# Optimization experiments

Measured on AMD Instinct MI355X. Metric: run time of the kernel, lower is better.

The kernel has to match this reference:

```python
import jax, jax.numpy as jnp
import numpy as np

N = 50000      # nodes
E = 800000     # edges (avg degree 16)
F_IN = 128     # input_dim
HID = 64       # hidden_dim
HEADS = 4      # heads on first layer only
G = 512        # number of graphs in batch
EPS = 1e-5
NEG_SLOPE = 0.2

# (in_dim, out_dim, heads) per GATv2 layer
LAYER_DIMS = [(F_IN, HID, HEADS), (HID * HEADS, HID, 1), (HID, HID, 1)]


def setup_inputs() -> dict:
    key = jax.random.key(0)
    ks = jax.random.split(key, 16)
    def rn(k, shape, fan_in):
        return jax.random.normal(k, shape, jnp.float32) / np.float32(np.sqrt(fan_in))
    inp = {}
    inp["x"] = jax.random.normal(ks[0], (N, F_IN), jnp.float32)
    inp["edge_index"] = jax.random.randint(ks[1], (2, E), 0, N)
    inp["batch"] = jnp.sort(jax.random.randint(ks[2], (N,), 0, G))
    i = 3
    for l, (din, dout, h) in enumerate(LAYER_DIMS):
        kk = jax.random.split(ks[i], 3)
        inp[f"Wl{l}"] = rn(kk[0], (din, h * dout), din)
        inp[f"bl{l}"] = jnp.zeros((h * dout,), jnp.float32)
        inp[f"Wr{l}"] = rn(kk[1], (din, h * dout), din)
        inp[f"br{l}"] = jnp.zeros((h * dout,), jnp.float32)
        inp[f"att{l}"] = rn(kk[2], (h, dout), dout)
        inp[f"bias{l}"] = jnp.zeros((h * dout,), jnp.float32)
        inp[f"ln_g{l}"] = jnp.ones((h * dout,), jnp.float32)
        inp[f"ln_b{l}"] = jnp.zeros((h * dout,), jnp.float32)
        i += 1
    inp["Wh1"] = rn(ks[i], (HID, HID), HID)
    inp["bh1"] = jnp.zeros((HID,), jnp.float32)
    inp["Wh2"] = rn(ks[i + 1], (HID, 1), HID)
    inp["bh2"] = jnp.zeros((1,), jnp.float32)
    return inp


def gatv2_layer(x, src, dst, Wl, bl, Wr, br, att, bias, heads, out_c):
    """PyG GATv2Conv (concat=True, share_weights=False, eval mode)."""
    n = x.shape[0]
    xl = (x @ Wl + bl).reshape(n, heads, out_c)   # messages (source side)
    xr = (x @ Wr + br).reshape(n, heads, out_c)   # destination side
    e = jax.nn.leaky_relu(xl[src] + xr[dst], NEG_SLOPE)          # [E,H,C]
    logit = jnp.einsum('ehc,hc->eh', e, att)                      # [E,H]
    m = jax.ops.segment_max(logit, dst, num_segments=n)           # segment-softmax
    ex = jnp.exp(logit - m[dst])
    den = jax.ops.segment_sum(ex, dst, num_segments=n)
    alpha = ex / den[dst]                                         # [E,H]
    out = jax.ops.segment_sum(alpha[:, :, None] * xl[src], dst, num_segments=n)
    return out.reshape(n, heads * out_c) + bias


def graph_layernorm(h, g, b):
    """PyG LayerNorm(mode='graph') with batch=None: normalize over all elements."""
    mu = h.mean()
    xc = h - mu
    var = (xc * xc).mean()
    return xc * jax.lax.rsqrt(var + EPS) * g + b


def reference(x, edge_index, batch,
              Wl0, bl0, Wr0, br0, att0, bias0, ln_g0, ln_b0,
              Wl1, bl1, Wr1, br1, att1, bias1, ln_g1, ln_b1,
              Wl2, bl2, Wr2, br2, att2, bias2, ln_g2, ln_b2,
              Wh1, bh1, Wh2, bh2):
    src, dst = edge_index[0], edge_index[1]
    layers = [
        (Wl0, bl0, Wr0, br0, att0, bias0, ln_g0, ln_b0),
        (Wl1, bl1, Wr1, br1, att1, bias1, ln_g1, ln_b1),
        (Wl2, bl2, Wr2, br2, att2, bias2, ln_g2, ln_b2),
    ]
    h = x
    for (Wl, bl, Wr, br, att, bias, g, b), (_, dout, heads) in zip(layers, LAYER_DIMS):
        h_in = h
        h = gatv2_layer(h, src, dst, Wl, bl, Wr, br, att, bias, heads, dout)
        h = graph_layernorm(h, g, b)
        h = jax.nn.relu(h)
        if h_in.shape[1] == h.shape[1]:   # residual only when widths match
            h = h + h_in
        # dropout: identity in eval mode
    # global mean pool over graphs
    counts = jax.ops.segment_sum(jnp.ones((h.shape[0], 1), h.dtype), batch, num_segments=G)
    Z = jax.ops.segment_sum(h, batch, num_segments=G) / jnp.maximum(counts, 1.0)
    logits = jax.nn.relu(Z @ Wh1 + bh1) @ Wh2 + bh2
    return logits
```

## Files before the change

### kernel.cpp

```cpp
#include <hip/hip_runtime.h>
#include <math.h>

#define NN 50000
#define NE 800000
#define NG 512
#define LRELU 0.2f
#define LN_EPS 1e-5
#define GCAP 128
#define NBUCK 256

typedef __attribute__((ext_vector_type(8))) short short8;
typedef __attribute__((ext_vector_type(4))) float f32x4;

__global__ void hist_kernel(const int* __restrict__ dst, int* __restrict__ deg) {
    int e = blockIdx.x * blockDim.x + threadIdx.x;
    if (e < NE) atomicAdd(&deg[dst[e]], 1);
}

__global__ __launch_bounds__(1024) void scan1(const int* __restrict__ deg,
                                              int* __restrict__ excl,
                                              int* __restrict__ bsum, int n) {
    __shared__ int s[1024];
    int tid = threadIdx.x;
    int gid = blockIdx.x * 1024 + tid;
    int v = (gid < n) ? deg[gid] : 0;
    s[tid] = v;
    __syncthreads();
    for (int off = 1; off < 1024; off <<= 1) {
        int t = (tid >= off) ? s[tid - off] : 0;
        __syncthreads();
        s[tid] += t;
        __syncthreads();
    }
    if (gid < n) excl[gid] = s[tid] - v;
    if (tid == 1023) bsum[blockIdx.x] = s[1023];
}

__global__ __launch_bounds__(64) void scan2(int* __restrict__ bsum, int nb) {
    int lane = threadIdx.x;
    int v = (lane < nb) ? bsum[lane] : 0;
    int orig = v;
    #pragma unroll
    for (int off = 1; off < 64; off <<= 1) {
        int t = __shfl_up(v, off, 64);
        if (lane >= off) v += t;
    }
    if (lane < nb) bsum[lane] = v - orig;
}

__global__ __launch_bounds__(1024) void scan3(int* __restrict__ row_ptr,
                                              int* __restrict__ cursor,
                                              const int* __restrict__ bsum, int n) {
    int tid = threadIdx.x;
    int gid = blockIdx.x * 1024 + tid;
    if (gid < n) {
        int v = row_ptr[gid] + bsum[blockIdx.x];
        row_ptr[gid] = v;
        cursor[gid] = v;
    }
    if (gid == 0) row_ptr[n] = NE;
}

__global__ void scatter_kernel(const int* __restrict__ src, const int* __restrict__ dst,
                               int* __restrict__ cursor, int* __restrict__ col_src) {
    int e = blockIdx.x * blockDim.x + threadIdx.x;
    if (e < NE) {
        int pos = atomicAdd(&cursor[dst[e]], 1);
        col_src[pos] = src[e];
    }
}

__device__ inline void split_bf16(float v, ushort& h, ushort& l) {
    unsigned ub = __float_as_uint(v);
    unsigned hh = (ub + 0x7FFFu + ((ub >> 16) & 1u)) >> 16;
    float vh = __uint_as_float(hh << 16);
    float r = v - vh;
    unsigned ur = __float_as_uint(r);
    unsigned ll = (ur + 0x7FFFu + ((ur >> 16) & 1u)) >> 16;
    h = (ushort)hh; l = (ushort)ll;
}

__global__ __launch_bounds__(256) void prep_w(const float* __restrict__ Wl0,
                                              const float* __restrict__ Wr0,
                                              const float* __restrict__ Wl1,
                                              const float* __restrict__ Wr1,
                                              const float* __restrict__ Wl2,
                                              const float* __restrict__ Wr2,
                                              ushort* __restrict__ wt) {
    int id = blockIdx.x * 256 + threadIdx.x;
    const float* W; int K, N, rel; ushort* hi;
    if (id < 65536) {
        W = (id < 32768) ? Wl0 : Wr0;
        rel = id & 32767; K = 128; N = 256;
        hi = wt + ((id < 32768) ? 0 : 65536);
    } else if (id < 98304) {
        int t = id - 65536;
        W = (t < 16384) ? Wl1 : Wr1;
        rel = t & 16383; K = 256; N = 64;
        hi = wt + 131072 + ((t < 16384) ? 0 : 32768);
    } else if (id < 106496) {
        int t = id - 98304;
        W = (t < 4096) ? Wl2 : Wr2;
        rel = t & 4095; K = 64; N = 64;
        hi = wt + 196608 + ((t < 4096) ? 0 : 8192);
    } else return;
    ushort* lo = hi + K * N;
    int n = rel / K, k = rel - n * K;
    ushort h, l;
    split_bf16(W[k * N + n], h, l);
    hi[rel] = h;
    lo[rel] = l;
}

__global__ __launch_bounds__(256) void gemm_mfma(const float* __restrict__ A,
                                                 const ushort* __restrict__ Bhi,
                                                 const ushort* __restrict__ Blo,
                                                 const float* __restrict__ bias,
                                                 float* __restrict__ C,
                                                 int M, int Ncol, int K,
                                                 const float* __restrict__ lnstats,
                                                 const float* __restrict__ lng,
                                                 const float* __restrict__ lnb) {
    __shared__ ushort sAh[64][40];
    __shared__ ushort sAl[64][40];
    __shared__ ushort sBh[64][40];
    __shared__ ushort sBl[64][40];
    const int tid = threadIdx.x;
    const int row0 = blockIdx.x * 64;
    const int col0 = blockIdx.y * 64;
    const int w = tid >> 6, lane = tid & 63;
    const int fm = lane & 15;
    const int fk = (lane >> 4) * 8;
    const bool doln = (lnstats != nullptr);
    float mu = 0.f, rstd = 0.f;
    if (doln) { mu = lnstats[0]; rstd = lnstats[1]; }
    f32x4 acc[4] = {};

    for (int k0 = 0; k0 < K; k0 += 32) {
        __syncthreads();
        int f = tid;
        #pragma unroll
        for (int it = 0; it < 2; it++, f += 256) {
            int r = f >> 3, kc = (f & 7) * 4;
            int grow = row0 + r;
            float4 v = (grow < M) ? *(const float4*)&A[(size_t)grow * K + k0 + kc]
                                  : make_float4(0.f, 0.f, 0.f, 0.f);
            if (doln) {
                int c0 = k0 + kc;
                v.x = fmaxf((v.x - mu) * rstd * lng[c0 + 0] + lnb[c0 + 0], 0.f);
                v.y = fmaxf((v.y - mu) * rstd * lng[c0 + 1] + lnb[c0 + 1], 0.f);
                v.z = fmaxf((v.z - mu) * rstd * lng[c0 + 2] + lnb[c0 + 2], 0.f);
                v.w = fmaxf((v.w - mu) * rstd * lng[c0 + 3] + lnb[c0 + 3], 0.f);
            }
            ushort4 h, l;
            split_bf16(v.x, h.x, l.x);
            split_bf16(v.y, h.y, l.y);
            split_bf16(v.z, h.z, l.z);
            split_bf16(v.w, h.w, l.w);
            *(ushort4*)&sAh[r][kc] = h;
            *(ushort4*)&sAl[r][kc] = l;
        }
        int u = tid;
        #pragma unroll
        for (int it = 0; it < 2; it++, u += 256) {
            int n = u >> 3, kc = (u & 7) * 4;
            *(ushort4*)&sBh[n][kc] = *(const ushort4*)&Bhi[(size_t)(col0 + n) * K + k0 + kc];
            *(ushort4*)&sBl[n][kc] = *(const ushort4*)&Blo[(size_t)(col0 + n) * K + k0 + kc];
        }
        __syncthreads();
        short8 ah = *(const short8*)&sAh[w * 16 + fm][fk];
        short8 al = *(const short8*)&sAl[w * 16 + fm][fk];
        #pragma unroll
        for (int c = 0; c < 4; c++) {
            short8 bh = *(const short8*)&sBh[c * 16 + fm][fk];
            short8 bl = *(const short8*)&sBl[c * 16 + fm][fk];
            acc[c] = __builtin_amdgcn_mfma_f32_16x16x32_bf16(ah, bh, acc[c], 0, 0, 0);
            acc[c] = __builtin_amdgcn_mfma_f32_16x16x32_bf16(al, bh, acc[c], 0, 0, 0);
            acc[c] = __builtin_amdgcn_mfma_f32_16x16x32_bf16(ah, bl, acc[c], 0, 0, 0);
        }
    }
    const int orow = w * 16 + (lane >> 4) * 4;
    #pragma unroll
    for (int c = 0; c < 4; c++) {
        int col = col0 + c * 16 + fm;
        float bv = bias[col];
        #pragma unroll
        for (int r = 0; r < 4; r++) {
            int grow = row0 + orow + r;
            if (grow < M) C[(size_t)grow * Ncol + col] = acc[c][r] + bv;
        }
    }
}

__global__ __launch_bounds__(256) void gat4(const float* __restrict__ xl,
                                            const float* __restrict__ xr,
                                            const float* __restrict__ att,
                                            const float* __restrict__ bias,
                                            const int* __restrict__ row_ptr,
                                            const int* __restrict__ col_src,
                                            float* __restrict__ out,
                                            double* __restrict__ red) {
    __shared__ int scol[4][GCAP];
    __shared__ double bs1[4], bs2[4];
    const int tid = threadIdx.x;
    const int w = tid >> 6, lane = tid & 63;
    const int n = blockIdx.x * 4 + w;
    const int base = row_ptr[n];
    int deg = row_ptr[n + 1] - base;
    if (deg > GCAP) deg = GCAP;
    for (int j = lane; j < deg; j += 64) scol[w][j] = col_src[base + j];
    const float4 rxr  = ((const float4*)(xr + (size_t)n * 256))[lane];
    const float4 ratt = ((const float4*)att)[lane];
    __syncthreads();

    float m = -1e30f, sum = 0.f;
    float4 acc = {0.f, 0.f, 0.f, 0.f};
    float4 xvn = {0.f, 0.f, 0.f, 0.f};
    if (deg > 0) xvn = ((const float4*)(xl + (size_t)scol[w][0] * 256))[lane];
    for (int j = 0; j < deg; j++) {
        float4 xv = xvn;
        if (j + 1 < deg) xvn = ((const float4*)(xl + (size_t)scol[w][j + 1] * 256))[lane];
        float vx = xv.x + rxr.x; vx = (vx > 0.f) ? vx : LRELU * vx;
        float vy = xv.y + rxr.y; vy = (vy > 0.f) ? vy : LRELU * vy;
        float vz = xv.z + rxr.z; vz = (vz > 0.f) ? vz : LRELU * vz;
        float vw = xv.w + rxr.w; vw = (vw > 0.f) ? vw : LRELU * vw;
        float p = vx * ratt.x + vy * ratt.y + vz * ratt.z + vw * ratt.w;
        p += __shfl_xor(p, 1, 64);
        p += __shfl_xor(p, 2, 64);
        p += __shfl_xor(p, 4, 64);
        p += __shfl_xor(p, 8, 64);
        float mn = fmaxf(m, p);
        float sc = __expf(m - mn);
        float e  = __expf(p - mn);
        sum = fmaf(sum, sc, e);
        acc.x = fmaf(acc.x, sc, e * xv.x);
        acc.y = fmaf(acc.y, sc, e * xv.y);
        acc.z = fmaf(acc.z, sc, e * xv.z);
        acc.w = fmaf(acc.w, sc, e * xv.w);
        m = mn;
    }
    float rden = (sum > 0.f) ? 1.f / sum : 0.f;
    float4 bv = ((const float4*)bias)[lane];
    float4 o;
    o.x = fmaf(acc.x, rden, bv.x);
    o.y = fmaf(acc.y, rden, bv.y);
    o.z = fmaf(acc.z, rden, bv.z);
    o.w = fmaf(acc.w, rden, bv.w);
    ((float4*)(out + (size_t)n * 256))[lane] = o;

    float s1 = o.x + o.y + o.z + o.w;
    float s2 = o.x * o.x + o.y * o.y + o.z * o.z + o.w * o.w;
    #pragma unroll
    for (int off = 32; off > 0; off >>= 1) {
        s1 += __shfl_xor(s1, off, 64);
        s2 += __shfl_xor(s2, off, 64);
    }
    if (lane == 0) { bs1[w] = (double)s1; bs2[w] = (double)s2; }
    __syncthreads();
    if (tid == 0) {
        double t1 = bs1[0] + bs1[1] + bs1[2] + bs1[3];
        double t2 = bs2[0] + bs2[1] + bs2[2] + bs2[3];
        int b = (blockIdx.x & (NBUCK - 1)) * 2;
        atomicAdd(&red[b], t1);
        atomicAdd(&red[b + 1], t2);
    }
}

__global__ __launch_bounds__(256) void gat1(const float* __restrict__ xl,
                                            const float* __restrict__ xr,
                                            const float* __restrict__ att,
                                            const float* __restrict__ bias,
                                            const int* __restrict__ row_ptr,
                                            const int* __restrict__ col_src,
                                            float* __restrict__ out,
                                            double* __restrict__ red) {
    __shared__ int scol[4][GCAP];
    __shared__ double bs1[4], bs2[4];
    const int tid = threadIdx.x;
    const int w = tid >> 6, lane = tid & 63;
    const int n = blockIdx.x * 4 + w;
    const int g = lane >> 4, li = lane & 15;
    const int base = row_ptr[n];
    int deg = row_ptr[n + 1] - base;
    if (deg > GCAP) deg = GCAP;
    for (int j = lane; j < deg; j += 64) scol[w][j] = col_src[base + j];
    const float4 rxr  = ((const float4*)(xr + (size_t)n * 64))[li];
    const float4 ratt = ((const float4*)att)[li];
    __syncthreads();

    float m = -1e30f, sum = 0.f;
    float4 acc = {0.f, 0.f, 0.f, 0.f};
    for (int j = g; j < deg; j += 4) {
        int s = scol[w][j];
        float4 xv = ((const float4*)(xl + (size_t)s * 64))[li];
        float vx = xv.x + rxr.x; vx = (vx > 0.f) ? vx : LRELU * vx;
        float vy = xv.y + rxr.y; vy = (vy > 0.f) ? vy : LRELU * vy;
        float vz = xv.z + rxr.z; vz = (vz > 0.f) ? vz : LRELU * vz;
        float vw = xv.w + rxr.w; vw = (vw > 0.f) ? vw : LRELU * vw;
        float p = vx * ratt.x + vy * ratt.y + vz * ratt.z + vw * ratt.w;
        p += __shfl_xor(p, 1, 64);
        p += __shfl_xor(p, 2, 64);
        p += __shfl_xor(p, 4, 64);
        p += __shfl_xor(p, 8, 64);
        float mn = fmaxf(m, p);
        float sc = __expf(m - mn);
        float e  = __expf(p - mn);
        sum = fmaf(sum, sc, e);
        acc.x = fmaf(acc.x, sc, e * xv.x);
        acc.y = fmaf(acc.y, sc, e * xv.y);
        acc.z = fmaf(acc.z, sc, e * xv.z);
        acc.w = fmaf(acc.w, sc, e * xv.w);
        m = mn;
    }
    #pragma unroll
    for (int off = 16; off < 64; off <<= 1) {
        float m2 = __shfl_xor(m, off, 64);
        float z2 = __shfl_xor(sum, off, 64);
        float ax = __shfl_xor(acc.x, off, 64);
        float ay = __shfl_xor(acc.y, off, 64);
        float az = __shfl_xor(acc.z, off, 64);
        float aw = __shfl_xor(acc.w, off, 64);
        float M = fmaxf(m, m2);
        float e1 = __expf(m - M), e2 = __expf(m2 - M);
        sum   = sum   * e1 + z2 * e2;
        acc.x = acc.x * e1 + ax * e2;
        acc.y = acc.y * e1 + ay * e2;
        acc.z = acc.z * e1 + az * e2;
        acc.w = acc.w * e1 + aw * e2;
        m = M;
    }
    float rden = (sum > 0.f) ? 1.f / sum : 0.f;
    float4 bv = ((const float4*)bias)[li];
    float4 o;
    o.x = fmaf(acc.x, rden, bv.x);
    o.y = fmaf(acc.y, rden, bv.y);
    o.z = fmaf(acc.z, rden, bv.z);
    o.w = fmaf(acc.w, rden, bv.w);
    if (g == 0) ((float4*)(out + (size_t)n * 64))[li] = o;

    float s1 = (g == 0) ? (o.x + o.y + o.z + o.w) : 0.f;
    float s2 = (g == 0) ? (o.x * o.x + o.y * o.y + o.z * o.z + o.w * o.w) : 0.f;
    #pragma unroll
    for (int off = 32; off > 0; off >>= 1) {
        s1 += __shfl_xor(s1, off, 64);
        s2 += __shfl_xor(s2, off, 64);
    }
    if (lane == 0) { bs1[w] = (double)s1; bs2[w] = (double)s2; }
    __syncthreads();
    if (tid == 0) {
        double t1 = bs1[0] + bs1[1] + bs1[2] + bs1[3];
        double t2 = bs2[0] + bs2[1] + bs2[2] + bs2[3];
        int b = (blockIdx.x & (NBUCK - 1)) * 2;
        atomicAdd(&red[b], t1);
        atomicAdd(&red[b + 1], t2);
    }
}

__global__ __launch_bounds__(NBUCK) void finalize_stats(const double* __restrict__ red,
                                                        float* __restrict__ stats, int M) {
    __shared__ double sa[NBUCK], sb[NBUCK];
    int t = threadIdx.x;
    sa[t] = red[t * 2];
    sb[t] = red[t * 2 + 1];
    __syncthreads();
    for (int off = NBUCK / 2; off > 0; off >>= 1) {
        if (t < off) { sa[t] += sa[t + off]; sb[t] += sb[t + off]; }
        __syncthreads();
    }
    if (t == 0) {
        double mu = sa[0] / M;
        double var = sb[0] / M - mu * mu;
        stats[0] = (float)mu;
        stats[1] = (float)(1.0 / sqrt(var + LN_EPS));
    }
}

__global__ void pool_ln(const float* __restrict__ C2, const float* __restrict__ D,
                        const float* __restrict__ stats,
                        const float* __restrict__ g1, const float* __restrict__ b1,
                        const float* __restrict__ g2, const float* __restrict__ b2,
                        const int* __restrict__ batch,
                        float* __restrict__ Zsum, int* __restrict__ gcount) {
    int i = blockIdx.x * blockDim.x + threadIdx.x;
    if (i >= NN * 64) return;
    int n = i >> 6, c = i & 63;
    float mu1 = stats[2], r1 = stats[3], mu2 = stats[4], r2 = stats[5];
    float hin = fmaxf((D[i] - mu1) * r1 * g1[c] + b1[c], 0.f);
    float v = fmaxf((C2[i] - mu2) * r2 * g2[c] + b2[c], 0.f) + hin;
    int gi = batch[n];
    atomicAdd(&Zsum[gi * 64 + c], v);
    if (c == 0) atomicAdd(&gcount[gi], 1);
}

__global__ __launch_bounds__(64) void mlp_head(const float* __restrict__ Zsum,
                                               const int* __restrict__ gcount,
                                               const float* __restrict__ Wh1,
                                               const float* __restrict__ bh1,
                                               const float* __restrict__ Wh2,
                                               const float* __restrict__ bh2,
                                               float* __restrict__ out) {
    __shared__ float sz[64];
    int g = blockIdx.x, tid = threadIdx.x;
    int cnt = gcount[g];
    float inv = 1.f / (float)(cnt > 1 ? cnt : 1);
    sz[tid] = Zsum[g * 64 + tid] * inv;
    __syncthreads();
    float acc = bh1[tid];
    #pragma unroll
    for (int c = 0; c < 64; c++) acc = fmaf(sz[c], Wh1[c * 64 + tid], acc);
    acc = fmaxf(acc, 0.f);
    float v = acc * Wh2[tid];
    #pragma unroll
    for (int off = 32; off > 0; off >>= 1) v += __shfl_xor(v, off, 64);
    if (tid == 0) out[g] = v + bh2[0];
}

extern "C" void kernel_launch(void* const* d_in, const int* in_sizes, int n_in,
                              void* d_out, int out_size, void* d_ws, size_t ws_size,
                              hipStream_t stream) {
    (void)in_sizes; (void)n_in; (void)out_size; (void)ws_size;
    const float* x     = (const float*)d_in[0];
    const int*   ei    = (const int*)d_in[1];
    const int*   batch = (const int*)d_in[2];
    const float* Wl0 = (const float*)d_in[3];  const float* bl0 = (const float*)d_in[4];
    const float* Wr0 = (const float*)d_in[5];  const float* br0 = (const float*)d_in[6];
    const float* at0 = (const float*)d_in[7];  const float* bi0 = (const float*)d_in[8];
    const float* lg0 = (const float*)d_in[9];  const float* lb0 = (const float*)d_in[10];
    const float* Wl1 = (const float*)d_in[11]; const float* bl1 = (const float*)d_in[12];
    const float* Wr1 = (const float*)d_in[13]; const float* br1 = (const float*)d_in[14];
    const float* at1 = (const float*)d_in[15]; const float* bi1 = (const float*)d_in[16];
    const float* lg1 = (const float*)d_in[17]; const float* lb1 = (const float*)d_in[18];
    const float* Wl2 = (const float*)d_in[19]; const float* bl2 = (const float*)d_in[20];
    const float* Wr2 = (const float*)d_in[21]; const float* br2 = (const float*)d_in[22];
    const float* at2 = (const float*)d_in[23]; const float* bi2 = (const float*)d_in[24];
    const float* lg2 = (const float*)d_in[25]; const float* lb2 = (const float*)d_in[26];
    const float* Wh1 = (const float*)d_in[27]; const float* bh1 = (const float*)d_in[28];
    const float* Wh2 = (const float*)d_in[29]; const float* bh2 = (const float*)d_in[30];
    float* out = (float*)d_out;

    const int* srcp = ei;
    const int* dstp = ei + NE;

    char* w = (char*)d_ws;
    size_t off = 0;
    auto carve = [&](size_t bytes) -> void* {
        void* p = w + off;
        off += (bytes + 255) & ~(size_t)255;
        return p;
    };
    float* A = (float*)carve((size_t)NN * 256 * 4);
    float* B = (float*)carve((size_t)NN * 256 * 4);
    float* C = (float*)carve((size_t)NN * 256 * 4);
    float* D = (float*)carve((size_t)NN * 64 * 4);
    ushort* wt = (ushort*)carve(212992 * 2);
    const size_t REDB = (size_t)3 * NBUCK * 2 * sizeof(double);
    size_t zbytes = REDB + (size_t)NG * 64 * 4 + NG * 4 + (size_t)NN * 4;
    char* zb = (char*)carve(zbytes);
    double* red   = (double*)zb;
    float*  Zsum  = (float*)(zb + REDB);
    int*    gcnt  = (int*)(zb + REDB + (size_t)NG * 64 * 4);
    int*    deg   = (int*)(zb + REDB + (size_t)NG * 64 * 4 + NG * 4);
    int* row_ptr = (int*)carve((size_t)(NN + 1) * 4);
    int* cursor  = (int*)carve((size_t)NN * 4);
    int* col_src = (int*)carve((size_t)NE * 4);
    int* bsum    = (int*)carve(64 * 4);
    float* stats = (float*)carve(6 * 4);

    const ushort* W0lh = wt;           const ushort* W0ll = wt + 32768;
    const ushort* W0rh = wt + 65536;   const ushort* W0rl = wt + 98304;
    const ushort* W1lh = wt + 131072;  const ushort* W1ll = wt + 147456;
    const ushort* W1rh = wt + 163840;  const ushort* W1rl = wt + 180224;
    const ushort* W2lh = wt + 196608;  const ushort* W2ll = wt + 200704;
    const ushort* W2rh = wt + 204800;  const ushort* W2rl = wt + 208896;

    hipMemsetAsync(zb, 0, zbytes, stream);
    prep_w<<<416, 256, 0, stream>>>(Wl0, Wr0, Wl1, Wr1, Wl2, Wr2, wt);

    hist_kernel<<<(NE + 255) / 256, 256, 0, stream>>>(dstp, deg);
    const int SB = (NN + 1023) / 1024;
    scan1<<<SB, 1024, 0, stream>>>(deg, row_ptr, bsum, NN);
    scan2<<<1, 64, 0, stream>>>(bsum, SB);
    scan3<<<SB, 1024, 0, stream>>>(row_ptr, cursor, bsum, NN);
    scatter_kernel<<<(NE + 255) / 256, 256, 0, stream>>>(srcp, dstp, cursor, col_src);

    const int GR = (NN + 63) / 64;
    const int GATB = NN / 4;

    gemm_mfma<<<dim3(GR, 4), 256, 0, stream>>>(x, W0lh, W0ll, bl0, A, NN, 256, 128,
                                               nullptr, nullptr, nullptr);
    gemm_mfma<<<dim3(GR, 4), 256, 0, stream>>>(x, W0rh, W0rl, br0, B, NN, 256, 128,
                                               nullptr, nullptr, nullptr);
    gat4<<<GATB, 256, 0, stream>>>(A, B, at0, bi0, row_ptr, col_src, C, red);
    finalize_stats<<<1, NBUCK, 0, stream>>>(red, stats, NN * 256);

    gemm_mfma<<<dim3(GR, 1), 256, 0, stream>>>(C, W1lh, W1ll, bl1, A, NN, 64, 256,
                                               stats, lg0, lb0);
    gemm_mfma<<<dim3(GR, 1), 256, 0, stream>>>(C, W1rh, W1rl, br1, B, NN, 64, 256,
                                               stats, lg0, lb0);
    gat1<<<GATB, 256, 0, stream>>>(A, B, at1, bi1, row_ptr, col_src, D, red + 2 * NBUCK);
    finalize_stats<<<1, NBUCK, 0, stream>>>(red + 2 * NBUCK, stats + 2, NN * 64);

    gemm_mfma<<<dim3(GR, 1), 256, 0, stream>>>(D, W2lh, W2ll, bl2, A, NN, 64, 64,
                                               stats + 2, lg1, lb1);
    gemm_mfma<<<dim3(GR, 1), 256, 0, stream>>>(D, W2rh, W2rl, br2, B, NN, 64, 64,
                                               stats + 2, lg1, lb1);
    gat1<<<GATB, 256, 0, stream>>>(A, B, at2, bi2, row_ptr, col_src, C, red + 4 * NBUCK);
    finalize_stats<<<1, NBUCK, 0, stream>>>(red + 4 * NBUCK, stats + 4, NN * 64);

    pool_ln<<<(NN * 64 + 255) / 256, 256, 0, stream>>>(C, D, stats, lg1, lb1, lg2, lb2,
                                                       batch, Zsum, gcnt);
    mlp_head<<<NG, 64, 0, stream>>>(Zsum, gcnt, Wh1, bh1, Wh2, bh2, out);
}
```

Measured before the change: 628.2 us.

## Merge paired GEMMs, fuse stats finalize into GAT, rework softmax loops and pooling

The left and right projection GEMMs of each layer now run in a single launch, selected by blockIdx.z. The separate finalize_stats kernels are removed: the last GAT block to finish, detected with an atomic counter, computes the LayerNorm statistics. The GAT inner loops switch to DPP reductions and deeper prefetch, and gat4 runs two interleaved online-softmax chains with a skip-rescale fast path. pool_ln becomes a per-wave segmented accumulation that issues far fewer atomics. The aim is to cut launch count, shuffle cost and atomic contention, at the cost of more complex code and a done-counter handshake.

After: 1.636 ms. 160% more time.

```diff
diff --git a/kernel.cpp b/kernel.cpp
--- a/kernel.cpp
+++ b/kernel.cpp
@@ -113,10 +113,14 @@
 }
 
 __global__ __launch_bounds__(256) void gemm_mfma(const float* __restrict__ A,
-                                                 const ushort* __restrict__ Bhi,
-                                                 const ushort* __restrict__ Blo,
-                                                 const float* __restrict__ bias,
-                                                 float* __restrict__ C,
+                                                 const ushort* __restrict__ Bh0,
+                                                 const ushort* __restrict__ Bl0,
+                                                 const float* __restrict__ bias0,
+                                                 float* __restrict__ C0,
+                                                 const ushort* __restrict__ Bh1,
+                                                 const ushort* __restrict__ Bl1,
+                                                 const float* __restrict__ bias1,
+                                                 float* __restrict__ C1,
                                                  int M, int Ncol, int K,
                                                  const float* __restrict__ lnstats,
                                                  const float* __restrict__ lng,
@@ -125,6 +129,10 @@
     __shared__ ushort sAl[64][40];
     __shared__ ushort sBh[64][40];
     __shared__ ushort sBl[64][40];
+    const ushort* Bhi = blockIdx.z ? Bh1 : Bh0;
+    const ushort* Blo = blockIdx.z ? Bl1 : Bl0;
+    const float*  bias = blockIdx.z ? bias1 : bias0;
+    float*        C = blockIdx.z ? C1 : C0;
     const int tid = threadIdx.x;
     const int row0 = blockIdx.x * 64;
     const int col0 = blockIdx.y * 64;
@@ -192,6 +200,67 @@
     }
 }
 
+__device__ inline float dpp_red_add16(float x) {
+    x += __int_as_float(__builtin_amdgcn_update_dpp(0, __float_as_int(x), 0xB1, 0xF, 0xF, true));
+    x += __int_as_float(__builtin_amdgcn_update_dpp(0, __float_as_int(x), 0x4E, 0xF, 0xF, true));
+    x += __int_as_float(__builtin_amdgcn_update_dpp(0, __float_as_int(x), 0x141, 0xF, 0xF, true));
+    x += __int_as_float(__builtin_amdgcn_update_dpp(0, __float_as_int(x), 0x140, 0xF, 0xF, true));
+    return x;
+}
+
+__device__ inline void gat_upd_fast(const float4& xv, const float4& rxr, const float4& ratt,
+                                    float& m, float& sum, float4& acc) {
+    float vx = xv.x + rxr.x; vx = fmaxf(vx, vx * LRELU);
+    float vy = xv.y + rxr.y; vy = fmaxf(vy, vy * LRELU);
+    float vz = xv.z + rxr.z; vz = fmaxf(vz, vz * LRELU);
+    float vw = xv.w + rxr.w; vw = fmaxf(vw, vw * LRELU);
+    float p = vx * ratt.x;
+    p = fmaf(vy, ratt.y, p);
+    p = fmaf(vz, ratt.z, p);
+    p = fmaf(vw, ratt.w, p);
+    p = dpp_red_add16(p);
+    if (__all(p <= m)) {
+        float e = __expf(p - m);
+        sum += e;
+        acc.x = fmaf(e, xv.x, acc.x);
+        acc.y = fmaf(e, xv.y, acc.y);
+        acc.z = fmaf(e, xv.z, acc.z);
+        acc.w = fmaf(e, xv.w, acc.w);
+    } else {
+        float mn = fmaxf(m, p);
+        float sc = __expf(m - mn);
+        float e  = __expf(p - mn);
+        sum = fmaf(sum, sc, e);
+        acc.x = fmaf(acc.x, sc, e * xv.x);
+        acc.y = fmaf(acc.y, sc, e * xv.y);
+        acc.z = fmaf(acc.z, sc, e * xv.z);
+        acc.w = fmaf(acc.w, sc, e * xv.w);
+        m = mn;
+    }
+}
+
+__device__ inline void gat_upd(const float4& xv, const float4& rxr, const float4& ratt,
+                               float& m, float& sum, float4& acc) {
+    float vx = xv.x + rxr.x; vx = fmaxf(vx, vx * LRELU);
+    float vy = xv.y + rxr.y; vy = fmaxf(vy, vy * LRELU);
+    float vz = xv.z + rxr.z; vz = fmaxf(vz, vz * LRELU);
+    float vw = xv.w + rxr.w; vw = fmaxf(vw, vw * LRELU);
+    float p = vx * ratt.x;
+    p = fmaf(vy, ratt.y, p);
+    p = fmaf(vz, ratt.z, p);
+    p = fmaf(vw, ratt.w, p);
+    p = dpp_red_add16(p);
+    float mn = fmaxf(m, p);
+    float sc = __expf(m - mn);
+    float e  = __expf(p - mn);
+    sum = fmaf(sum, sc, e);
+    acc.x = fmaf(acc.x, sc, e * xv.x);
+    acc.y = fmaf(acc.y, sc, e * xv.y);
+    acc.z = fmaf(acc.z, sc, e * xv.z);
+    acc.w = fmaf(acc.w, sc, e * xv.w);
+    m = mn;
+}
+
 __global__ __launch_bounds__(256) void gat4(const float* __restrict__ xl,
                                             const float* __restrict__ xr,
                                             const float* __restrict__ att,
@@ -199,9 +268,13 @@
                                             const int* __restrict__ row_ptr,
                                             const int* __restrict__ col_src,
                                             float* __restrict__ out,
-                                            double* __restrict__ red) {
+                                            double* __restrict__ red,
+                                            float* __restrict__ stats,
+                                            unsigned int* __restrict__ done,
+                                            int Mdiv) {
     __shared__ int scol[4][GCAP];
     __shared__ double bs1[4], bs2[4];
+    __shared__ int slast;
     const int tid = threadIdx.x;
     const int w = tid >> 6, lane = tid & 63;
     const int n = blockIdx.x * 4 + w;
@@ -213,32 +286,32 @@
     const float4 ratt = ((const float4*)att)[lane];
     __syncthreads();
 
-    float m = -1e30f, sum = 0.f;
-    float4 acc = {0.f, 0.f, 0.f, 0.f};
-    float4 xvn = {0.f, 0.f, 0.f, 0.f};
-    if (deg > 0) xvn = ((const float4*)(xl + (size_t)scol[w][0] * 256))[lane];
-    for (int j = 0; j < deg; j++) {
-        float4 xv = xvn;
-        if (j + 1 < deg) xvn = ((const float4*)(xl + (size_t)scol[w][j + 1] * 256))[lane];
-        float vx = xv.x + rxr.x; vx = (vx > 0.f) ? vx : LRELU * vx;
-        float vy = xv.y + rxr.y; vy = (vy > 0.f) ? vy : LRELU * vy;
-        float vz = xv.z + rxr.z; vz = (vz > 0.f) ? vz : LRELU * vz;
-        float vw = xv.w + rxr.w; vw = (vw > 0.f) ? vw : LRELU * vw;
-        float p = vx * ratt.x + vy * ratt.y + vz * ratt.z + vw * ratt.w;
-        p += __shfl_xor(p, 1, 64);
-        p += __shfl_xor(p, 2, 64);
-        p += __shfl_xor(p, 4, 64);
-        p += __shfl_xor(p, 8, 64);
-        float mn = fmaxf(m, p);
-        float sc = __expf(m - mn);
-        float e  = __expf(p - mn);
-        sum = fmaf(sum, sc, e);
-        acc.x = fmaf(acc.x, sc, e * xv.x);
-        acc.y = fmaf(acc.y, sc, e * xv.y);
-        acc.z = fmaf(acc.z, sc, e * xv.z);
-        acc.w = fmaf(acc.w, sc, e * xv.w);
-        m = mn;
-    }
+    float m0 = -1e30f, s0 = 0.f, m1 = -1e30f, s1 = 0.f;
+    float4 a0 = {0.f, 0.f, 0.f, 0.f}, a1 = {0.f, 0.f, 0.f, 0.f};
+    if (deg > 0) {
+        const int dm1 = deg - 1;
+        auto L = [&](int j) {
+            int idx = (j < dm1) ? j : dm1;
+            return ((const float4*)(xl + (size_t)scol[w][idx] * 256))[lane];
+        };
+        float4 b0 = L(0), b1 = L(1), b2 = L(2), b3 = L(3);
+        for (int j = 0; j < deg; j += 2) {
+            float4 x0 = b0, x1 = b1;
+            b0 = b2; b1 = b3;
+            b2 = L(j + 4); b3 = L(j + 5);
+            gat_upd_fast(x0, rxr, ratt, m0, s0, a0);
+            if (j + 1 < deg) gat_upd_fast(x1, rxr, ratt, m1, s1, a1);
+        }
+    }
+    float M = fmaxf(m0, m1);
+    float e0 = __expf(m0 - M), e1 = __expf(m1 - M);
+    float sum = s0 * e0 + s1 * e1;
+    float4 acc;
+    acc.x = a0.x * e0 + a1.x * e1;
+    acc.y = a0.y * e0 + a1.y * e1;
+    acc.z = a0.z * e0 + a1.z * e1;
+    acc.w = a0.w * e0 + a1.w * e1;
+
     float rden = (sum > 0.f) ? 1.f / sum : 0.f;
     float4 bv = ((const float4*)bias)[lane];
     float4 o;
@@ -248,14 +321,14 @@
     o.w = fmaf(acc.w, rden, bv.w);
     ((float4*)(out + (size_t)n * 256))[lane] = o;
 
-    float s1 = o.x + o.y + o.z + o.w;
-    float s2 = o.x * o.x + o.y * o.y + o.z * o.z + o.w * o.w;
+    float z1 = o.x + o.y + o.z + o.w;
+    float z2 = o.x * o.x + o.y * o.y + o.z * o.z + o.w * o.w;
     #pragma unroll
     for (int off = 32; off > 0; off >>= 1) {
-        s1 += __shfl_xor(s1, off, 64);
-        s2 += __shfl_xor(s2, off, 64);
-    }
-    if (lane == 0) { bs1[w] = (double)s1; bs2[w] = (double)s2; }
+        z1 += __shfl_xor(z1, off, 64);
+        z2 += __shfl_xor(z2, off, 64);
+    }
+    if (lane == 0) { bs1[w] = (double)z1; bs2[w] = (double)z2; }
     __syncthreads();
     if (tid == 0) {
         double t1 = bs1[0] + bs1[1] + bs1[2] + bs1[3];
@@ -263,6 +336,29 @@
         int b = (blockIdx.x & (NBUCK - 1)) * 2;
         atomicAdd(&red[b], t1);
         atomicAdd(&red[b + 1], t2);
+        __threadfence();
+        unsigned prev = atomicAdd(done, 1u);
+        slast = (prev == (unsigned)(gridDim.x - 1));
+    }
+    __syncthreads();
+    if (slast) {
+        double va = atomicAdd(&red[tid * 2], 0.0);
+        double vb = atomicAdd(&red[tid * 2 + 1], 0.0);
+        #pragma unroll
+        for (int off = 32; off > 0; off >>= 1) {
+            va += __shfl_xor(va, off, 64);
+            vb += __shfl_xor(vb, off, 64);
+        }
+        if (lane == 0) { bs1[w] = va; bs2[w] = vb; }
+        __syncthreads();
+        if (tid == 0) {
+            double t1 = bs1[0] + bs1[1] + bs1[2] + bs1[3];
+            double t2 = bs2[0] + bs2[1] + bs2[2] + bs2[3];
+            double mu = t1 / Mdiv;
+            double var = t2 / Mdiv - mu * mu;
+            stats[0] = (float)mu;
+            stats[1] = (float)(1.0 / sqrt(var + LN_EPS));
+        }
     }
 }
 
@@ -273,9 +369,13 @@
                                             const int* __restrict__ row_ptr,
                                             const int* __restrict__ col_src,
                                             float* __restrict__ out,
-                                            double* __restrict__ red) {
+                                            double* __restrict__ red,
+                                            float* __restrict__ stats,
+                                            unsigned int* __restrict__ done,
+                                            int Mdiv) {
     __shared__ int scol[4][GCAP];
     __shared__ double bs1[4], bs2[4];
+    __shared__ int slast;
     const int tid = threadIdx.x;
     const int w = tid >> 6, lane = tid & 63;
     const int n = blockIdx.x * 4 + w;
@@ -290,27 +390,18 @@
 
     float m = -1e30f, sum = 0.f;
     float4 acc = {0.f, 0.f, 0.f, 0.f};
-    for (int j = g; j < deg; j += 4) {
-        int s = scol[w][j];
-        float4 xv = ((const float4*)(xl + (size_t)s * 64))[li];
-        float vx = xv.x + rxr.x; vx = (vx > 0.f) ? vx : LRELU * vx;
-        float vy = xv.y + rxr.y; vy = (vy > 0.f) ? vy : LRELU * vy;
-        float vz = xv.z + rxr.z; vz = (vz > 0.f) ? vz : LRELU * vz;
-        float vw = xv.w + rxr.w; vw = (vw > 0.f) ? vw : LRELU * vw;
-        float p = vx * ratt.x + vy * ratt.y + vz * ratt.z + vw * ratt.w;
-        p += __shfl_xor(p, 1, 64);
-        p += __shfl_xor(p, 2, 64);
-        p += __shfl_xor(p, 4, 64);
-        p += __shfl_xor(p, 8, 64);
-        float mn = fmaxf(m, p);
-        float sc = __expf(m - mn);
-        float e  = __expf(p - mn);
-        sum = fmaf(sum, sc, e);
-        acc.x = fmaf(acc.x, sc, e * xv.x);
-        acc.y = fmaf(acc.y, sc, e * xv.y);
-        acc.z = fmaf(acc.z, sc, e * xv.z);
-        acc.w = fmaf(acc.w, sc, e * xv.w);
-        m = mn;
+    if (deg > 0) {
+        const int dm1 = deg - 1;
+        auto Lg = [&](int j) {
+            int idx = (j < dm1) ? j : dm1;
+            return ((const float4*)(xl + (size_t)scol[w][idx] * 64))[li];
+        };
+        float4 xvn = Lg(g);
+        for (int j = g; j < deg; j += 4) {
+            float4 xv = xvn;
+            xvn = Lg(j + 4);
+            gat_upd(xv, rxr, ratt, m, sum, acc);
+        }
     }
     #pragma unroll
     for (int off = 16; off < 64; off <<= 1) {
@@ -338,14 +429,14 @@
     o.w = fmaf(acc.w, rden, bv.w);
     if (g == 0) ((float4*)(out + (size_t)n * 64))[li] = o;
 
-    float s1 = (g == 0) ? (o.x + o.y + o.z + o.w) : 0.f;
-    float s2 = (g == 0) ? (o.x * o.x + o.y * o.y + o.z * o.z + o.w * o.w) : 0.f;
+    float z1 = (g == 0) ? (o.x + o.y + o.z + o.w) : 0.f;
+    float z2 = (g == 0) ? (o.x * o.x + o.y * o.y + o.z * o.z + o.w * o.w) : 0.f;
     #pragma unroll
     for (int off = 32; off > 0; off >>= 1) {
-        s1 += __shfl_xor(s1, off, 64);
-        s2 += __shfl_xor(s2, off, 64);
-    }
-    if (lane == 0) { bs1[w] = (double)s1; bs2[w] = (double)s2; }
+        z1 += __shfl_xor(z1, off, 64);
+        z2 += __shfl_xor(z2, off, 64);
+    }
+    if (lane == 0) { bs1[w] = (double)z1; bs2[w] = (double)z2; }
     __syncthreads();
     if (tid == 0) {
         double t1 = bs1[0] + bs1[1] + bs1[2] + bs1[3];
@@ -353,43 +444,67 @@
         int b = (blockIdx.x & (NBUCK - 1)) * 2;
         atomicAdd(&red[b], t1);
         atomicAdd(&red[b + 1], t2);
-    }
-}
-
-__global__ __launch_bounds__(NBUCK) void finalize_stats(const double* __restrict__ red,
-                                                        float* __restrict__ stats, int M) {
-    __shared__ double sa[NBUCK], sb[NBUCK];
-    int t = threadIdx.x;
-    sa[t] = red[t * 2];
-    sb[t] = red[t * 2 + 1];
-    __syncthreads();
-    for (int off = NBUCK / 2; off > 0; off >>= 1) {
-        if (t < off) { sa[t] += sa[t + off]; sb[t] += sb[t + off]; }
+        __threadfence();
+        unsigned prev = atomicAdd(done, 1u);
+        slast = (prev == (unsigned)(gridDim.x - 1));
+    }
+    __syncthreads();
+    if (slast) {
+        double va = atomicAdd(&red[tid * 2], 0.0);
+        double vb = atomicAdd(&red[tid * 2 + 1], 0.0);
+        #pragma unroll
+        for (int off = 32; off > 0; off >>= 1) {
+            va += __shfl_xor(va, off, 64);
+            vb += __shfl_xor(vb, off, 64);
+        }
+        if (lane == 0) { bs1[w] = va; bs2[w] = vb; }
         __syncthreads();
-    }
-    if (t == 0) {
-        double mu = sa[0] / M;
-        double var = sb[0] / M - mu * mu;
-        stats[0] = (float)mu;
-        stats[1] = (float)(1.0 / sqrt(var + LN_EPS));
-    }
-}
-
-__global__ void pool_ln(const float* __restrict__ C2, const float* __restrict__ D,
-                        const float* __restrict__ stats,
-                        const float* __restrict__ g1, const float* __restrict__ b1,
-                        const float* __restrict__ g2, const float* __restrict__ b2,
-                        const int* __restrict__ batch,
-                        float* __restrict__ Zsum, int* __restrict__ gcount) {
-    int i = blockIdx.x * blockDim.x + threadIdx.x;
-    if (i >= NN * 64) return;
-    int n = i >> 6, c = i & 63;
-    float mu1 = stats[2], r1 = stats[3], mu2 = stats[4], r2 = stats[5];
-    float hin = fmaxf((D[i] - mu1) * r1 * g1[c] + b1[c], 0.f);
-    float v = fmaxf((C2[i] - mu2) * r2 * g2[c] + b2[c], 0.f) + hin;
-    int gi = batch[n];
-    atomicAdd(&Zsum[gi * 64 + c], v);
-    if (c == 0) atomicAdd(&gcount[gi], 1);
+        if (tid == 0) {
+            double t1 = bs1[0] + bs1[1] + bs1[2] + bs1[3];
+            double t2 = bs2[0] + bs2[1] + bs2[2] + bs2[3];
+            double mu = t1 / Mdiv;
+            double var = t2 / Mdiv - mu * mu;
+            stats[0] = (float)mu;
+            stats[1] = (float)(1.0 / sqrt(var + LN_EPS));
+        }
+    }
+}
+
+#define PLB 256
+__global__ __launch_bounds__(256) void pool_ln(const float* __restrict__ C2,
+                                               const float* __restrict__ D,
+                                               const float* __restrict__ stats,
+                                               const float* __restrict__ g1,
+                                               const float* __restrict__ b1,
+                                               const float* __restrict__ g2,
+                                               const float* __restrict__ b2,
+                                               const int* __restrict__ batch,
+                                               float* __restrict__ Zsum,
+                                               int* __restrict__ gcount) {
+    const int wid = blockIdx.x * 4 + (threadIdx.x >> 6);
+    const int lane = threadIdx.x & 63;
+    const int NW = PLB * 4;
+    const int per = (NN + NW - 1) / NW;
+    int n0 = wid * per;
+    int n1 = n0 + per; if (n1 > NN) n1 = NN;
+    if (n0 >= n1) return;
+    const float mu1 = stats[2], r1 = stats[3], mu2 = stats[4], r2 = stats[5];
+    const float ga = r1 * g1[lane], ba = fmaf(-mu1, ga, b1[lane]);
+    const float gb = r2 * g2[lane], bb = fmaf(-mu2, gb, b2[lane]);
+    float zacc = 0.f; int cnt = 0; int cur = batch[n0];
+    for (int n = n0; n < n1; n++) {
+        int gi = batch[n];
+        if (gi != cur) {
+            atomicAdd(&Zsum[cur * 64 + lane], zacc);
+            if (lane == 0) atomicAdd(&gcount[cur], cnt);
+            zacc = 0.f; cnt = 0; cur = gi;
+        }
+        float hin = fmaxf(fmaf(D[(size_t)n * 64 + lane], ga, ba), 0.f);
+        float v = fmaxf(fmaf(C2[(size_t)n * 64 + lane], gb, bb), 0.f) + hin;
+        zacc += v; cnt++;
+    }
+    atomicAdd(&Zsum[cur * 64 + lane], zacc);
+    if (lane == 0) atomicAdd(&gcount[cur], cnt);
 }
 
 __global__ __launch_bounds__(64) void mlp_head(const float* __restrict__ Zsum,
@@ -454,12 +569,13 @@
     float* D = (float*)carve((size_t)NN * 64 * 4);
     ushort* wt = (ushort*)carve(212992 * 2);
     const size_t REDB = (size_t)3 * NBUCK * 2 * sizeof(double);
-    size_t zbytes = REDB + (size_t)NG * 64 * 4 + NG * 4 + (size_t)NN * 4;
+    size_t zbytes = REDB + (size_t)NG * 64 * 4 + NG * 4 + (size_t)NN * 4 + 64;
     char* zb = (char*)carve(zbytes);
     double* red   = (double*)zb;
     float*  Zsum  = (float*)(zb + REDB);
     int*    gcnt  = (int*)(zb + REDB + (size_t)NG * 64 * 4);
     int*    deg   = (int*)(zb + REDB + (size_t)NG * 64 * 4 + NG * 4);
+    unsigned int* done = (unsigned int*)(zb + REDB + (size_t)NG * 64 * 4 + NG * 4 + (size_t)NN * 4);
     int* row_ptr = (int*)carve((size_t)(NN + 1) * 4);
     int* cursor  = (int*)carve((size_t)NN * 4);
     int* col_src = (int*)carve((size_t)NE * 4);
@@ -486,28 +602,25 @@
     const int GR = (NN + 63) / 64;
     const int GATB = NN / 4;
 
-    gemm_mfma<<<dim3(GR, 4), 256, 0, stream>>>(x, W0lh, W0ll, bl0, A, NN, 256, 128,
-                                               nullptr, nullptr, nullptr);
-    gemm_mfma<<<dim3(GR, 4), 256, 0, stream>>>(x, W0rh, W0rl, br0, B, NN, 256, 128,
-                                               nullptr, nullptr, nullptr);
-    gat4<<<GATB, 256, 0, stream>>>(A, B, at0, bi0, row_ptr, col_src, C, red);
-    finalize_stats<<<1, NBUCK, 0, stream>>>(red, stats, NN * 256);
-
-    gemm_mfma<<<dim3(GR, 1), 256, 0, stream>>>(C, W1lh, W1ll, bl1, A, NN, 64, 256,
-                                               stats, lg0, lb0);
-    gemm_mfma<<<dim3(GR, 1), 256, 0, stream>>>(C, W1rh, W1rl, br1, B, NN, 64, 256,
-                                               stats, lg0, lb0);
-    gat1<<<GATB, 256, 0, stream>>>(A, B, at1, bi1, row_ptr, col_src, D, red + 2 * NBUCK);
-    finalize_stats<<<1, NBUCK, 0, stream>>>(red + 2 * NBUCK, stats + 2, NN * 64);
-
-    gemm_mfma<<<dim3(GR, 1), 256, 0, stream>>>(D, W2lh, W2ll, bl2, A, NN, 64, 64,
-                                               stats + 2, lg1, lb1);
-    gemm_mfma<<<dim3(GR, 1), 256, 0, stream>>>(D, W2rh, W2rl, br2, B, NN, 64, 64,
-                                               stats + 2, lg1, lb1);
-    gat1<<<GATB, 256, 0, stream>>>(A, B, at2, bi2, row_ptr, col_src, C, red + 4 * NBUCK);
-    finalize_stats<<<1, NBUCK, 0, stream>>>(red + 4 * NBUCK, stats + 4, NN * 64);
-
-    pool_ln<<<(NN * 64 + 255) / 256, 256, 0, stream>>>(C, D, stats, lg1, lb1, lg2, lb2,
-                                                       batch, Zsum, gcnt);
+    gemm_mfma<<<dim3(GR, 4, 2), 256, 0, stream>>>(x, W0lh, W0ll, bl0, A,
+                                                  W0rh, W0rl, br0, B, NN, 256, 128,
+                                                  nullptr, nullptr, nullptr);
+    gat4<<<GATB, 256, 0, stream>>>(A, B, at0, bi0, row_ptr, col_src, C,
+                                   red, stats, done + 0, NN * 256);
+
+    gemm_mfma<<<dim3(GR, 1, 2), 256, 0, stream>>>(C, W1lh, W1ll, bl1, A,
+                                                  W1rh, W1rl, br1, B, NN, 64, 256,
+                                                  stats, lg0, lb0);
+    gat1<<<GATB, 256, 0, stream>>>(A, B, at1, bi1, row_ptr, col_src, D,
+                                   red + 2 * NBUCK, stats + 2, done + 1, NN * 64);
+
+    gemm_mfma<<<dim3(GR, 1, 2), 256, 0, stream>>>(D, W2lh, W2ll, bl2, A,
+                                                  W2rh, W2rl, br2, B, NN, 64, 64,
+                                                  stats + 2, lg1, lb1);
+    gat1<<<GATB, 256, 0, stream>>>(A, B, at2, bi2, row_ptr, col_src, C,
+                                   red + 4 * NBUCK, stats + 4, done + 2, NN * 64);
+
+    pool_ln<<<PLB, 256, 0, stream>>>(C, D, stats, lg1, lb1, lg2, lb2,
+                                     batch, Zsum, gcnt);
     mlp_head<<<NG, 64, 0, stream>>>(Zsum, gcnt, Wh1, bh1, Wh2, bh2, out);
 }
```
